# Optimization experiments

Measured on AMD Instinct MI355X. Metric: run time of the kernel, lower is better.

## Reference

```python
import jax, jax.numpy as jnp
import numpy as np

B, N, T = 128, 4096, 64


def setup_inputs() -> dict:
    key = jax.random.key(0)
    k1, k2, k3 = jax.random.split(key, 3)
    x = jax.random.normal(k1, (B, N, T), dtype=jnp.float32)
    # Vth init: uniform(Vth - range/2, Vth + range/2) with Vth=0.5, range=0 -> constant 0.5;
    # keep a small spread for numerical generality
    Vth = 0.5 + 0.0 * jax.random.uniform(k2, (N,), dtype=jnp.float32)
    # tau init: uniform around 0.7
    tau = 0.7 + 0.0 * jax.random.uniform(k3, (N,), dtype=jnp.float32)
    return {"x": x, "Vth": Vth, "tau": tau}


def reference(x, Vth, tau):
    # constrain_method == 'forward'
    Vth_c = jnp.maximum(Vth, 0.0)          # [N]
    tau_c = jnp.clip(tau, 0.0, 1.0)        # [N]

    xs = jnp.moveaxis(x, -1, 0)            # [T, B, N] time-major for scan
    u0 = jnp.zeros(x.shape[:-1], x.dtype)  # init_u == 'zero'
    o0 = jnp.zeros_like(u0)                # out[..., max(-1,0)] is zeros at step 0

    def step(carry, x_t):
        u, o = carry
        # reset_by_subtraction: u' = tau*(u - Vth*o) + x_t ; zoned_out == 1
        u_new = tau_c * (u - Vth_c * o) + x_t
        o_new = (u_new - Vth_c > 0.0).astype(x.dtype)  # SpikeAct forward: heaviside
        return (u_new, o_new), o_new

    _, outs = jax.lax.scan(step, (u0, o0), xs)  # outs: [T, B, N]
    return jnp.moveaxis(outs, 0, -1)            # [B, N, T]
```

## Files before the change

### kernel.cpp

```cpp
#include <hip/hip_runtime.h>


constexpr int B = 128;
constexpr int N = 4096;
constexpr int T = 64;
constexpr int ROWS = 256;
constexpr int TILE_WORDS = ROWS * T;

__global__ __launch_bounds__(256) void lif_spike_kernel(
    const float* __restrict__ x,
    const float* __restrict__ Vth,
    const float* __restrict__ tau,
    float* __restrict__ out)
{
    __shared__ float lds[TILE_WORDS];

    const int tid = threadIdx.x;
    const long long tile_base = (long long)blockIdx.x * TILE_WORDS;

    #pragma unroll
    for (int k = 0; k < 64; ++k) {
        const int widx = k * 256 + tid;
        const int row  = widx >> 6;
        const int t    = widx & 63;
        lds[(row << 6) | (t ^ (row & 31))] = x[tile_base + widx];
    }
    __syncthreads();

    {
        const long long grow = (long long)blockIdx.x * ROWS + tid;
        const int n = (int)(grow & (N - 1));

        const float vth = fmaxf(Vth[n], 0.0f);
        const float tc  = fminf(fmaxf(tau[n], 0.0f), 1.0f);

        float u = 0.0f, o = 0.0f;
        const int base = tid << 6;
        const int c    = tid & 31;
        #pragma unroll
        for (int t = 0; t < 64; ++t) {
            const int idx = base | (t ^ c);
            const float xt = lds[idx];
            u = tc * (u - vth * o) + xt;
            o = (u > vth) ? 1.0f : 0.0f;
            lds[idx] = o;
        }
    }
    __syncthreads();

    #pragma unroll
    for (int k = 0; k < 64; ++k) {
        const int widx = k * 256 + tid;
        const int row  = widx >> 6;
        const int t    = widx & 63;
        out[tile_base + widx] = lds[(row << 6) | (t ^ (row & 31))];
    }
}

extern "C" void kernel_launch(void* const* d_in, const int* in_sizes, int n_in,
                              void* d_out, int out_size, void* d_ws, size_t ws_size,
                              hipStream_t stream) {
    const float* x   = (const float*)d_in[0];
    const float* Vth = (const float*)d_in[1];
    const float* tau = (const float*)d_in[2];
    float* out       = (float*)d_out;

    const int grid = (B * N) / ROWS;
    lif_spike_kernel<<<grid, 256, 0, stream>>>(x, Vth, tau, out);
}
```

Measured before the change: 48.88 us.

## Load input rows directly as float4 and stage outputs through chunked LDS

Each thread now loads its own 64-element row straight from global memory as float4 vectors into registers, instead of staging the whole input tile through shared memory. Outputs are written into a smaller 16-column LDS chunk and flushed with coalesced stores after each chunk. This shrinks LDS from 64KB to 16KB, which should raise occupancy and remove one LDS round trip. The cost is per-thread strided global loads, which are less coalesced across the wavefront, plus higher register pressure from 64 floats per thread and extra barriers.

```diff
diff --git a/kernel.cpp b/kernel.cpp
--- a/kernel.cpp
+++ b/kernel.cpp
@@ -5,7 +5,8 @@
 constexpr int N = 4096;
 constexpr int T = 64;
 constexpr int ROWS = 256;
-constexpr int TILE_WORDS = ROWS * T;
+constexpr int CH = 16;
+constexpr int NCH = T / CH;
 
 __global__ __launch_bounds__(256) void lif_spike_kernel(
     const float* __restrict__ x,
@@ -13,47 +14,52 @@
     const float* __restrict__ tau,
     float* __restrict__ out)
 {
-    __shared__ float lds[TILE_WORDS];
+    __shared__ float lds[ROWS * CH];
 
     const int tid = threadIdx.x;
-    const long long tile_base = (long long)blockIdx.x * TILE_WORDS;
+    const long long row0 = (long long)blockIdx.x * ROWS;
+    const long long grow = row0 + tid;
+    const int n = (int)(grow & (N - 1));
+
+    const float vth = fmaxf(Vth[n], 0.0f);
+    const float tc  = fminf(fmaxf(tau[n], 0.0f), 1.0f);
+
+    const float4* __restrict__ xp = reinterpret_cast<const float4*>(x + grow * T);
+    float4 xv[T / 4];
+    #pragma unroll
+    for (int j = 0; j < T / 4; ++j) xv[j] = xp[j];
+
+    const int wbase = tid * CH;
+    const int wswz  = (tid >> 1) & 15;
+
+    float u = 0.0f, o = 0.0f;
+    const long long tile_word = row0 * T;
 
     #pragma unroll
-    for (int k = 0; k < 64; ++k) {
-        const int widx = k * 256 + tid;
-        const int row  = widx >> 6;
-        const int t    = widx & 63;
-        lds[(row << 6) | (t ^ (row & 31))] = x[tile_base + widx];
-    }
-    __syncthreads();
+    for (int c = 0; c < NCH; ++c) {
+        #pragma unroll
+        for (int q = 0; q < 4; ++q) {
+            const float4 xx = xv[c * 4 + q];
+            u = tc * (u - vth * o) + xx.x; o = (u > vth) ? 1.0f : 0.0f;
+            lds[wbase + ((q * 4 + 0) ^ wswz)] = o;
+            u = tc * (u - vth * o) + xx.y; o = (u > vth) ? 1.0f : 0.0f;
+            lds[wbase + ((q * 4 + 1) ^ wswz)] = o;
+            u = tc * (u - vth * o) + xx.z; o = (u > vth) ? 1.0f : 0.0f;
+            lds[wbase + ((q * 4 + 2) ^ wswz)] = o;
+            u = tc * (u - vth * o) + xx.w; o = (u > vth) ? 1.0f : 0.0f;
+            lds[wbase + ((q * 4 + 3) ^ wswz)] = o;
+        }
+        __syncthreads();
 
-    {
-        const long long grow = (long long)blockIdx.x * ROWS + tid;
-        const int n = (int)(grow & (N - 1));
-
-        const float vth = fmaxf(Vth[n], 0.0f);
-        const float tc  = fminf(fmaxf(tau[n], 0.0f), 1.0f);
-
-        float u = 0.0f, o = 0.0f;
-        const int base = tid << 6;
-        const int c    = tid & 31;
         #pragma unroll
-        for (int t = 0; t < 64; ++t) {
-            const int idx = base | (t ^ c);
-            const float xt = lds[idx];
-            u = tc * (u - vth * o) + xt;
-            o = (u > vth) ? 1.0f : 0.0f;
-            lds[idx] = o;
+        for (int k2 = 0; k2 < 16; ++k2) {
+            const int widx = k2 * 256 + tid;
+            const int row  = widx >> 4;
+            const int t    = widx & 15;
+            const float v  = lds[row * CH + (t ^ ((row >> 1) & 15))];
+            out[tile_word + (long long)row * T + c * CH + t] = v;
         }
-    }
-    __syncthreads();
-
-    #pragma unroll
-    for (int k = 0; k < 64; ++k) {
-        const int widx = k * 256 + tid;
-        const int row  = widx >> 6;
-        const int t    = widx & 63;
-        out[tile_base + widx] = lds[(row << 6) | (t ^ (row & 31))];
+        __syncthreads();
     }
 }
 
```

New measurement: 57.55 us. 1.18x slower.
